# Kernel optimization log

Hardware: AMD Instinct MI355X
Metric: run time of the kernel (lower is better)

Reference implementation:

```python
import jax, jax.numpy as jnp
import numpy as np

L, K, HID, OUT, B, N, E = 2, 3, 64, 32, 8, 10000, 160000


def setup_inputs() -> dict:
    key = jax.random.key(0)
    ks = jax.random.split(key, 12)
    s = 0.05
    return {
        "edge_weight": jax.random.uniform(ks[1], (E,), dtype=jnp.float32),
        "hidden_states": jax.random.normal(ks[2], (L, B, N, HID), dtype=jnp.float32),
        "go_input": jax.random.normal(ks[3], (B, N, HID), dtype=jnp.float32),
        "Wz": jax.random.normal(ks[4], (L, 2, K, 2 * HID, HID), dtype=jnp.float32) * s,
        "bz": jnp.zeros((L, HID), dtype=jnp.float32),
        "Wr": jax.random.normal(ks[5], (L, 2, K, 2 * HID, HID), dtype=jnp.float32) * s,
        "br": jnp.zeros((L, HID), dtype=jnp.float32),
        "Wh": jax.random.normal(ks[6], (L, 2, K, 2 * HID, HID), dtype=jnp.float32) * s,
        "bh": jnp.zeros((L, HID), dtype=jnp.float32),
        "proj_W": jax.random.normal(ks[7], (HID, OUT), dtype=jnp.float32) * s,
        "proj_b": jnp.zeros((OUT,), dtype=jnp.float32),
        "edge_index": jax.random.randint(ks[0], (2, E), 0, N, dtype=jnp.int32),
    }


def _prop(z, s_idx, d_idx, nw):
    # z: [B,N,F]; aggregate nw-weighted source features at destinations
    m = z[:, s_idx, :] * nw[None, :, None]  # [B,E,F]
    return jnp.zeros_like(z).at[:, d_idx, :].add(m)


def _dconv(x, W, b, src, dst, norm_out, norm_in):
    # x: [B,N,Fin]; W: [2,K,Fin,Fout] (dir 0 = forward walk, dir 1 = reverse)
    H = jnp.einsum('bnf,fo->bno', x, W[0, 0] + W[1, 0])  # T0 shared
    To_pp, Ti_pp = x, x
    To_p = _prop(x, src, dst, norm_out)
    Ti_p = _prop(x, dst, src, norm_in)
    H = H + jnp.einsum('bnf,fo->bno', To_p, W[0, 1]) + jnp.einsum('bnf,fo->bno', Ti_p, W[1, 1])
    for k in range(2, K):  # Chebyshev recursion over hops
        To = 2.0 * _prop(To_p, src, dst, norm_out) - To_pp
        Ti = 2.0 * _prop(Ti_p, dst, src, norm_in) - Ti_pp
        H = H + jnp.einsum('bnf,fo->bno', To, W[0, k]) + jnp.einsum('bnf,fo->bno', Ti, W[1, k])
        To_pp, To_p = To_p, To
        Ti_pp, Ti_p = Ti_p, Ti
    return H + b


def _cell(x, h, Wz, bz, Wr, br, Wh, bh, src, dst, no, ni):
    xh = jnp.concatenate([x, h], axis=-1)
    Z = jax.nn.sigmoid(_dconv(xh, Wz, bz, src, dst, no, ni))
    R = jax.nn.sigmoid(_dconv(xh, Wr, br, src, dst, no, ni))
    Ht = jnp.tanh(_dconv(jnp.concatenate([x, R * h], axis=-1), Wh, bh, src, dst, no, ni))
    return Z * h + (1.0 - Z) * Ht


def reference(edge_weight, hidden_states, go_input, Wz, bz, Wr, br, Wh, bh, proj_W, proj_b, edge_index):
    src, dst = edge_index[0], edge_index[1]
    deg_out = jax.ops.segment_sum(edge_weight, src, num_segments=N)
    deg_in = jax.ops.segment_sum(edge_weight, dst, num_segments=N)
    inv_out = 1.0 / jnp.where(deg_out > 0, deg_out, 1.0)
    inv_in = 1.0 / jnp.where(deg_in > 0, deg_in, 1.0)
    norm_out = edge_weight * inv_out[src]
    norm_in = edge_weight * inv_in[dst]

    cur = go_input
    last = cur
    for l in range(L):  # small fixed layer loop (dropout=0 -> identity)
        last = _cell(cur, hidden_states[l], Wz[l], bz[l], Wr[l], br[l], Wh[l], bh[l],
                     src, dst, norm_out, norm_in)
        if l < L - 1:
            cur = last
    return jnp.einsum('bnh,ho->bno', last, proj_W) + proj_b
```

## Files before the change

### kernel.cpp

```cpp
#include <hip/hip_runtime.h>
#include <math.h>

#define NL 2
#define KK 3
#define HIDD 64
#define OUTD 32
#define NB 8
#define NN 10000
#define NE 160000
#define ROWS 80000
#define WSTRIDE (128*HIDD)

typedef __attribute__((ext_vector_type(8))) short bf16x8;
typedef __attribute__((ext_vector_type(8))) unsigned short u16x8;
typedef __attribute__((ext_vector_type(4))) unsigned short u16x4;
typedef __attribute__((ext_vector_type(4))) float f32x4;

__device__ __forceinline__ ushort f2b(float x) {
    union { float f; unsigned u; } v; v.f = x;
    unsigned r = (v.u + 0x7fff + ((v.u >> 16) & 1)) >> 16;
    return (ushort)r;
}
__device__ __forceinline__ float b2f(ushort u) {
    union { unsigned u; float f; } v; v.u = (unsigned)u << 16;
    return v.f;
}

__global__ void zero_kernel(int* p, long n) {
    long t = (long)blockIdx.x * blockDim.x + threadIdx.x;
    if (t < n) p[t] = 0;
}

__global__ void deg_cnt_kernel(const float* __restrict__ w, const int* __restrict__ src,
                               const int* __restrict__ dst, float* deg_out, float* deg_in,
                               int* cnt_f, int* cnt_r) {
    int e = blockIdx.x * blockDim.x + threadIdx.x;
    if (e >= NE) return;
    int s = src[e], d = dst[e];
    float we = w[e];
    atomicAdd(&deg_out[s], we);
    atomicAdd(&deg_in[d], we);
    atomicAdd(&cnt_f[d], 1);
    atomicAdd(&cnt_r[s], 1);
}

__global__ void scan_kernel(const int* __restrict__ cnt, int* __restrict__ off) {
    __shared__ int part[256];
    const int CH = (NN + 255) / 256;
    int t = threadIdx.x;
    int s = 0;
    for (int i = 0; i < CH; ++i) {
        int idx = t * CH + i;
        if (idx < NN) s += cnt[idx];
    }
    part[t] = s;
    __syncthreads();
    if (t == 0) {
        int run = 0;
        for (int i = 0; i < 256; ++i) { int v = part[i]; part[i] = run; run += v; }
        off[NN] = run;
    }
    __syncthreads();
    int run = part[t];
    for (int i = 0; i < CH; ++i) {
        int idx = t * CH + i;
        if (idx < NN) { off[idx] = run; run += cnt[idx]; }
    }
}

__global__ void copy_pos_kernel(const int* __restrict__ off_f, const int* __restrict__ off_r,
                                int* pos_f, int* pos_r) {
    int t = blockIdx.x * blockDim.x + threadIdx.x;
    if (t < NN) { pos_f[t] = off_f[t]; pos_r[t] = off_r[t]; }
}

__global__ void fill_kernel(const float* __restrict__ w, const int* __restrict__ src,
                            const int* __restrict__ dst, const float* __restrict__ deg_out,
                            const float* __restrict__ deg_in,
                            int* pos_f, int* pos_r,
                            int* col_f, float* w_f, int* col_r, float* w_r) {
    int e = blockIdx.x * blockDim.x + threadIdx.x;
    if (e >= NE) return;
    int s = src[e], d = dst[e];
    float we = w[e];
    float dgo = deg_out[s]; dgo = (dgo > 0.f) ? dgo : 1.f;
    float dgi = deg_in[d];  dgi = (dgi > 0.f) ? dgi : 1.f;
    int pf = atomicAdd(&pos_f[d], 1);
    col_f[pf] = s; w_f[pf] = we / dgo;
    int pr = atomicAdd(&pos_r[s], 1);
    col_r[pr] = d; w_r[pr] = we / dgi;
}

__global__ void convW_kernel(const float* __restrict__ Wz, const float* __restrict__ Wr,
                             const float* __restrict__ Wh, ushort* __restrict__ Wt) {
    int t = blockIdx.x * 256 + threadIdx.x;
    if (t >= 2 * 3 * 2 * 3 * 64 * 128) return;
    int f = t & 127;
    int r1 = t >> 7;
    int o = r1 & 63;
    int r2 = r1 >> 6;
    int k = r2 % 3;
    int r3 = r2 / 3;
    int d = r3 & 1;
    int r4 = r3 >> 1;
    int g = r4 % 3;
    int l = r4 / 3;
    const float* W = (g == 0) ? Wz : (g == 1) ? Wr : Wh;
    float v = W[(((long)(l * 2 + d) * 3 + k) * 128 + f) * 64 + o];
    if (k == 0 && d == 0)
        v += W[(((long)(l * 2 + 1) * 3 + 0) * 128 + f) * 64 + o];
    Wt[t] = f2b(v);
}

__global__ void convX_perm(const float* __restrict__ in, ushort* __restrict__ xh, int c,
                           float* __restrict__ hp) {
    long t = (long)blockIdx.x * blockDim.x + threadIdx.x;
    if (t >= (long)ROWS * 16) return;
    int q = (int)(t & 15);
    long rowin = t >> 4;
    int b = (int)(rowin / NN);
    int n = (int)(rowin - (long)b * NN);
    f32x4 v = __builtin_nontemporal_load((const f32x4*)&in[t * 4]);
    u16x4 r;
    r.x = f2b(v.x); r.y = f2b(v.y); r.z = f2b(v.z); r.w = f2b(v.w);
    long orow = (long)n * 8 + b;
    *(u16x4*)&xh[orow * 128 + c * 64 + q * 4] = r;
    if (hp) *(f32x4*)&hp[orow * 64 + q * 4] = v;
}

struct PropCfg {
    const ushort* X[2];
    const ushort* base[2];
    const int*    off[2];
    const int*    col[2];
    const float*  w[2];
    ushort*       out[2];
};

template<int HALF, int NDIR>
__global__ __launch_bounds__(128) void prop_slice(PropCfg C, float alpha, float beta) {
    constexpr int LPG = HALF ? 8 : 16;
    constexpr int GPB = 128 / LPG;
    int bid = blockIdx.x;
    int b = bid & 7;
    int r = bid >> 3;
    int dir, tile;
    if (NDIR == 2) { dir = r & 1; tile = r >> 1; }
    else           { dir = 0;     tile = r; }
    int g    = threadIdx.x / LPG;
    int lane = threadIdx.x % LPG;
    int n = tile * GPB + g;
    const ushort* X   = C.X[dir];
    const ushort* bas = C.base[dir];
    const int*    off = C.off[dir];
    const int*    col = C.col[dir];
    const float*  w   = C.w[dir];
    ushort*       out = C.out[dir];
    int s = off[n], e = off[n + 1];
    int eo = b * 128 + (HALF ? 64 : 0) + lane * 8;
    float acc[8];
    #pragma unroll
    for (int i = 0; i < 8; ++i) acc[i] = 0.f;
    int j = s;
    for (; j + 2 <= e; j += 2) {
        int c0 = col[j], c1 = col[j + 1];
        float w0 = w[j], w1 = w[j + 1];
        u16x8 v0 = *(const u16x8*)&X[(long)c0 * 1024 + eo];
        u16x8 v1 = *(const u16x8*)&X[(long)c1 * 1024 + eo];
        #pragma unroll
        for (int i = 0; i < 8; ++i) acc[i] = fmaf(b2f(v0[i]), w0, acc[i]);
        #pragma unroll
        for (int i = 0; i < 8; ++i) acc[i] = fmaf(b2f(v1[i]), w1, acc[i]);
    }
    if (j < e) {
        int c = col[j];
        float ww = w[j];
        u16x8 v = *(const u16x8*)&X[(long)c * 1024 + eo];
        #pragma unroll
        for (int i = 0; i < 8; ++i) acc[i] = fmaf(b2f(v[i]), ww, acc[i]);
    }
    long o = (long)n * 1024 + eo;
    #pragma unroll
    for (int i = 0; i < 8; ++i) acc[i] *= alpha;
    if (beta != 0.f) {
        u16x8 bb = *(const u16x8*)&bas[o];
        #pragma unroll
        for (int i = 0; i < 8; ++i) acc[i] = fmaf(beta, b2f(bb[i]), acc[i]);
    }
    u16x8 rr;
    #pragma unroll
    for (int i = 0; i < 8; ++i) rr[i] = f2b(acc[i]);
    *(u16x8*)&out[o] = rr;
}

struct GM {
    const ushort* X[10];
    const ushort* Wa[10];
    const ushort* Wb[10];
};

#define LOADF(tt, aa, bb)                                                          \
    {                                                                              \
        const ushort* Xp = A.X[tt];                                                \
        const ushort* Wp = gate ? A.Wb[tt] : A.Wa[tt];                             \
        _Pragma("unroll")                                                          \
        for (int ks = 0; ks < 2; ++ks) {                                           \
            _Pragma("unroll")                                                      \
            for (int mi = 0; mi < 2; ++mi)                                         \
                aa[ks][mi] = *(const bf16x8*)&Xp[(grow + mi * 16 + lr) * 128 +     \
                                                 ks * 32 + lk * 8];                \
            _Pragma("unroll")                                                      \
            for (int ni = 0; ni < 4; ++ni)                                         \
                bb[ks][ni] = *(const bf16x8*)&Wp[(ni * 16 + lr) * 128 +            \
                                                 ks * 32 + lk * 8];                \
        }                                                                          \
    }

#define MFMAF(aa, bb)                                                              \
    _Pragma("unroll")                                                              \
    for (int ks = 0; ks < 2; ++ks)                                                 \
        _Pragma("unroll")                                                          \
        for (int mi = 0; mi < 2; ++mi)                                             \
            _Pragma("unroll")                                                      \
            for (int ni = 0; ni < 4; ++ni)                                         \
                acc[mi][ni] = __builtin_amdgcn_mfma_f32_16x16x32_bf16(             \
                    aa[ks][mi], bb[ks][ni], acc[mi][ni], 0, 0, 0);

template<int NT>
__global__ __launch_bounds__(256, 4) void mfma_dual(GM A,
        const float* __restrict__ bzp, const float* __restrict__ brp,
        const float* __restrict__ hp,
        float* __restrict__ Z, ushort* __restrict__ xh) {
    int lane = threadIdx.x & 63;
    int wid  = threadIdx.x >> 6;
    int gate = wid >> 1;
    long grow = (long)blockIdx.x * 64 + (long)(wid & 1) * 32;
    int lr = lane & 15;
    int lk = lane >> 4;
    f32x4 acc[2][4];
    #pragma unroll
    for (int i = 0; i < 2; ++i)
        #pragma unroll
        for (int j = 0; j < 4; ++j)
            acc[i][j] = (f32x4){0.f, 0.f, 0.f, 0.f};

    bf16x8 a0[2][2], b0[2][4], a1[2][2], b1[2][4];
    LOADF(0, a0, b0);
    #pragma unroll
    for (int tt = 0; tt < NT; tt += 2) {
        if (tt + 1 < NT) LOADF(tt + 1, a1, b1);
        MFMAF(a0, b0);
        if (tt + 2 < NT) LOADF(tt + 2, a0, b0);
        if (tt + 1 < NT) MFMAF(a1, b1);
    }

    const float* bias = gate ? brp : bzp;
    #pragma unroll
    for (int mi = 0; mi < 2; ++mi) {
        #pragma unroll
        for (int q = 0; q < 4; ++q) {
            long row = grow + mi * 16 + lk * 4 + q;
            #pragma unroll
            for (int ni = 0; ni < 4; ++ni) {
                int colc = ni * 16 + lr;
                float v = acc[mi][ni][q] + bias[colc];
                float sg = 1.f / (1.f + expf(-v));
                if (gate == 0) {
                    Z[row * 64 + colc] = sg;
                } else {
                    float hv = hp[row * 64 + colc];
                    xh[row * 128 + 64 + colc] = f2b(sg * hv);
                }
            }
        }
    }
}

template<int NT>
__global__ __launch_bounds__(128, 4) void mfma_single(GM A,
        const float* __restrict__ bhp, const float* __restrict__ hp,
        const float* __restrict__ Zg,
        float* __restrict__ outF, ushort* __restrict__ xh, int writeF) {
    int lane = threadIdx.x & 63;
    int wid  = threadIdx.x >> 6;
    const int gate = 0;
    long grow = (long)blockIdx.x * 64 + (long)wid * 32;
    int lr = lane & 15;
    int lk = lane >> 4;
    f32x4 acc[2][4];
    #pragma unroll
    for (int i = 0; i < 2; ++i)
        #pragma unroll
        for (int j = 0; j < 4; ++j)
            acc[i][j] = (f32x4){0.f, 0.f, 0.f, 0.f};

    bf16x8 a0[2][2], b0[2][4], a1[2][2], b1[2][4];
    LOADF(0, a0, b0);
    #pragma unroll
    for (int tt = 0; tt < NT; tt += 2) {
        if (tt + 1 < NT) LOADF(tt + 1, a1, b1);
        MFMAF(a0, b0);
        if (tt + 2 < NT) LOADF(tt + 2, a0, b0);
        if (tt + 1 < NT) MFMAF(a1, b1);
    }

    #pragma unroll
    for (int mi = 0; mi < 2; ++mi) {
        #pragma unroll
        for (int q = 0; q < 4; ++q) {
            long row = grow + mi * 16 + lk * 4 + q;
            #pragma unroll
            for (int ni = 0; ni < 4; ++ni) {
                int colc = ni * 16 + lr;
                float v = acc[mi][ni][q] + bhp[colc];
                float ht = tanhf(v);
                float z = Zg[row * 64 + colc];
                float hv = hp[row * 64 + colc];
                float res = z * hv + (1.f - z) * ht;
                if (writeF) outF[row * 64 + colc] = res;
                else        xh[row * 128 + colc] = f2b(res);
            }
        }
    }
}

__global__ void proj_kernel(const float* __restrict__ last, const float* __restrict__ W,
                            const float* __restrict__ bias, float* __restrict__ out) {
    long t = (long)blockIdx.x * blockDim.x + threadIdx.x;
    if (t >= (long)ROWS * OUTD) return;
    long row = t >> 5;
    int  o   = (int)(t & 31);
    int n = (int)(row >> 3), b = (int)(row & 7);
    float acc = bias[o];
    #pragma unroll
    for (int hh = 0; hh < HIDD; ++hh)
        acc = fmaf(last[row * 64 + hh], W[hh * OUTD + o], acc);
    out[((long)b * NN + n) * 32 + o] = acc;
}

extern "C" void kernel_launch(void* const* d_in, const int* in_sizes, int n_in,
                              void* d_out, int out_size, void* d_ws, size_t ws_size,
                              hipStream_t stream) {
    const float* edge_weight = (const float*)d_in[0];
    const float* hidden      = (const float*)d_in[1];
    const float* go_input    = (const float*)d_in[2];
    const float* Wz = (const float*)d_in[3];
    const float* bz = (const float*)d_in[4];
    const float* Wr = (const float*)d_in[5];
    const float* br = (const float*)d_in[6];
    const float* Wh = (const float*)d_in[7];
    const float* bh = (const float*)d_in[8];
    const float* projW = (const float*)d_in[9];
    const float* projb = (const float*)d_in[10];
    const int*   eidx  = (const int*)d_in[11];
    const int* src = eidx;
    const int* dst = eidx + NE;
    float* out = (float*)d_out;

    char* p = (char*)d_ws;
    auto alloc = [&](size_t bytes) { char* r = p; p += (bytes + 15) & ~(size_t)15; return r; };
    float* deg_out = (float*)alloc(NN * 4);
    float* deg_in  = (float*)alloc(NN * 4);
    int*   cnt_f   = (int*)alloc(NN * 4);
    int*   cnt_r   = (int*)alloc(NN * 4);
    int*   off_f   = (int*)alloc((NN + 4) * 4);
    int*   off_r   = (int*)alloc((NN + 4) * 4);
    int*   pos_f   = (int*)alloc(NN * 4);
    int*   pos_r   = (int*)alloc(NN * 4);
    int*   col_f   = (int*)alloc(NE * 4);
    float* w_f     = (float*)alloc(NE * 4);
    int*   col_r   = (int*)alloc(NE * 4);
    float* w_r     = (float*)alloc(NE * 4);
    ushort* Wt     = (ushort*)alloc((size_t)2 * 3 * 2 * 3 * 64 * 128 * 2);
    const size_t XB = (size_t)ROWS * 128 * 2;
    ushort* xh  = (ushort*)alloc(XB);
    ushort* Tf1 = (ushort*)alloc(XB);
    ushort* Tf2 = (ushort*)alloc(XB);
    ushort* Tr1 = (ushort*)alloc(XB);
    ushort* Tr2 = (ushort*)alloc(XB);
    float*  Zbuf = (float*)alloc((size_t)ROWS * HIDD * 4);
    float*  hp   = (float*)alloc((size_t)ROWS * HIDD * 4);
    if ((size_t)(p - (char*)d_ws) > ws_size) return;

    const int TB = 256;
    const int EGRID = (NE + TB - 1) / TB;

    zero_kernel<<<(4 * NN + TB - 1) / TB, TB, 0, stream>>>((int*)deg_out, 4 * NN);
    deg_cnt_kernel<<<EGRID, TB, 0, stream>>>(edge_weight, src, dst, deg_out, deg_in, cnt_f, cnt_r);
    scan_kernel<<<1, 256, 0, stream>>>(cnt_f, off_f);
    scan_kernel<<<1, 256, 0, stream>>>(cnt_r, off_r);
    copy_pos_kernel<<<(NN + TB - 1) / TB, TB, 0, stream>>>(off_f, off_r, pos_f, pos_r);
    fill_kernel<<<EGRID, TB, 0, stream>>>(edge_weight, src, dst, deg_out, deg_in,
                                          pos_f, pos_r, col_f, w_f, col_r, w_r);

    convW_kernel<<<2304, 256, 0, stream>>>(Wz, Wr, Wh, Wt);
    convX_perm<<<5000, 256, 0, stream>>>(go_input, xh, 0, nullptr);

    auto wt_term = [&](int l, int g, int d, int k, int c) -> const ushort* {
        return Wt + ((((long)((l * 3 + g) * 2 + d) * 3 + k) * 64) * 128) + (long)c * 64;
    };
    const int dd[5]  = {0, 0, 0, 1, 1};
    const int kk2[5] = {0, 1, 2, 1, 2};

    for (int l = 0; l < NL; ++l) {
        const float* h = hidden + (long)l * ROWS * HIDD;
        convX_perm<<<5000, 256, 0, stream>>>(h, xh, 1, hp);

        {
            PropCfg c1{};
            c1.X[0] = xh;  c1.off[0] = off_f; c1.col[0] = col_f; c1.w[0] = w_f; c1.out[0] = Tf1;
            c1.X[1] = xh;  c1.off[1] = off_r; c1.col[1] = col_r; c1.w[1] = w_r; c1.out[1] = Tr1;
            prop_slice<0, 2><<<(NN / 8) * 2 * 8, 128, 0, stream>>>(c1, 1.f, 0.f);
            PropCfg c2f{};
            c2f.X[0] = Tf1; c2f.base[0] = xh;
            c2f.off[0] = off_f; c2f.col[0] = col_f; c2f.w[0] = w_f; c2f.out[0] = Tf2;
            prop_slice<0, 1><<<(NN / 8) * 8, 128, 0, stream>>>(c2f, 2.f, -1.f);
            PropCfg c2r{};
            c2r.X[0] = Tr1; c2r.base[0] = xh;
            c2r.off[0] = off_r; c2r.col[0] = col_r; c2r.w[0] = w_r; c2r.out[0] = Tr2;
            prop_slice<0, 1><<<(NN / 8) * 8, 128, 0, stream>>>(c2r, 2.f, -1.f);
        }

        const ushort* xs[5] = {xh, Tf1, Tf2, Tr1, Tr2};
        GM A{};
        for (int i = 0; i < 5; ++i) {
            A.X[i]      = xs[i];
            A.X[5 + i]  = xs[i] + 64;
            A.Wa[i]     = wt_term(l, 0, dd[i], kk2[i], 0);
            A.Wa[5 + i] = wt_term(l, 0, dd[i], kk2[i], 1);
            A.Wb[i]     = wt_term(l, 1, dd[i], kk2[i], 0);
            A.Wb[5 + i] = wt_term(l, 1, dd[i], kk2[i], 1);
        }
        mfma_dual<10><<<ROWS / 64, 256, 0, stream>>>(A, bz + l * HIDD, br + l * HIDD,
                                                     hp, Zbuf, xh);

        {
            PropCfg c1{};
            c1.X[0] = xh;  c1.off[0] = off_f; c1.col[0] = col_f; c1.w[0] = w_f; c1.out[0] = Tf1;
            c1.X[1] = xh;  c1.off[1] = off_r; c1.col[1] = col_r; c1.w[1] = w_r; c1.out[1] = Tr1;
            prop_slice<1, 2><<<(NN / 16) * 2 * 8, 128, 0, stream>>>(c1, 1.f, 0.f);
            PropCfg c2{};
            c2.X[0] = Tf1; c2.base[0] = xh;
            c2.off[0] = off_f; c2.col[0] = col_f; c2.w[0] = w_f; c2.out[0] = Tf2;
            c2.X[1] = Tr1; c2.base[1] = xh;
            c2.off[1] = off_r; c2.col[1] = col_r; c2.w[1] = w_r; c2.out[1] = Tr2;
            prop_slice<1, 2><<<(NN / 16) * 2 * 8, 128, 0, stream>>>(c2, 2.f, -1.f);
        }

        GM Ah{};
        for (int i = 0; i < 5; ++i) {
            Ah.X[i]      = xs[i];
            Ah.X[5 + i]  = xs[i] + 64;
            Ah.Wa[i]     = wt_term(l, 2, dd[i], kk2[i], 0);
            Ah.Wa[5 + i] = wt_term(l, 2, dd[i], kk2[i], 1);
        }
        mfma_single<10><<<ROWS / 64, 128, 0, stream>>>(Ah, bh + l * HIDD, hp, Zbuf,
                                                       Zbuf, xh, (l == NL - 1) ? 1 : 0);
    }

    proj_kernel<<<(int)(((long)ROWS * OUTD + TB - 1) / TB), TB, 0, stream>>>(
        Zbuf, projW, projb, out);
}
```

Measured before the change: 960.9 us.

## Sort graph nodes by degree for load-balanced propagation and enlarge dual GEMM tile

Adds a per-direction degree histogram, a scan and a scatter that build a permutation of nodes sorted by in-degree. The propagation kernels then map each thread group to a permuted node, so groups in a block have similar edge counts and less lane divergence. Separately, the dual-gate MFMA kernel now processes 128 rows per block (64 per wave) with launch bounds lowered to 2 blocks per CU, reusing weight fragments across more rows at the cost of more registers and lower occupancy. The extra setup kernels add a small fixed cost, and sorting by degree scatters output writes and source rows.

```diff
diff --git a/kernel.cpp b/kernel.cpp
--- a/kernel.cpp
+++ b/kernel.cpp
@@ -10,6 +10,7 @@
 #define NE 160000
 #define ROWS 80000
 #define WSTRIDE (128*HIDD)
+#define MAXD 512
 
 typedef __attribute__((ext_vector_type(8))) short bf16x8;
 typedef __attribute__((ext_vector_type(8))) unsigned short u16x8;
@@ -89,6 +90,24 @@
     col_f[pf] = s; w_f[pf] = we / dgo;
     int pr = atomicAdd(&pos_r[s], 1);
     col_r[pr] = d; w_r[pr] = we / dgi;
+}
+
+__global__ void hist_kernel(const int* __restrict__ deg, int* hist) {
+    int n = blockIdx.x * blockDim.x + threadIdx.x;
+    if (n < NN) atomicAdd(&hist[min(deg[n], MAXD - 1)], 1);
+}
+__global__ void scan512_kernel(const int* __restrict__ hist, int* boff) {
+    if (threadIdx.x == 0) {
+        int run = 0;
+        for (int i = 0; i < MAXD; ++i) { boff[i] = run; run += hist[i]; }
+    }
+}
+__global__ void scatter_perm_kernel(const int* __restrict__ deg, int* boff, int* perm) {
+    int n = blockIdx.x * blockDim.x + threadIdx.x;
+    if (n < NN) {
+        int pos = atomicAdd(&boff[min(deg[n], MAXD - 1)], 1);
+        perm[pos] = n;
+    }
 }
 
 __global__ void convW_kernel(const float* __restrict__ Wz, const float* __restrict__ Wr,
@@ -134,6 +153,7 @@
     const int*    off[2];
     const int*    col[2];
     const float*  w[2];
+    const int*    perm[2];
     ushort*       out[2];
 };
 
@@ -149,7 +169,7 @@
     else           { dir = 0;     tile = r; }
     int g    = threadIdx.x / LPG;
     int lane = threadIdx.x % LPG;
-    int n = tile * GPB + g;
+    int n = C.perm[dir][tile * GPB + g];
     const ushort* X   = C.X[dir];
     const ushort* bas = C.base[dir];
     const int*    off = C.off[dir];
@@ -199,14 +219,14 @@
     const ushort* Wb[10];
 };
 
-#define LOADF(tt, aa, bb)                                                          \
+#define LOADF4(tt, aa, bb)                                                         \
     {                                                                              \
         const ushort* Xp = A.X[tt];                                                \
         const ushort* Wp = gate ? A.Wb[tt] : A.Wa[tt];                             \
         _Pragma("unroll")                                                          \
         for (int ks = 0; ks < 2; ++ks) {                                           \
             _Pragma("unroll")                                                      \
-            for (int mi = 0; mi < 2; ++mi)                                         \
+            for (int mi = 0; mi < 4; ++mi)                                         \
                 aa[ks][mi] = *(const bf16x8*)&Xp[(grow + mi * 16 + lr) * 128 +     \
                                                  ks * 32 + lk * 8];                \
             _Pragma("unroll")                                                      \
@@ -216,47 +236,47 @@
         }                                                                          \
     }
 
-#define MFMAF(aa, bb)                                                              \
+#define MFMAF4(aa, bb)                                                             \
     _Pragma("unroll")                                                              \
     for (int ks = 0; ks < 2; ++ks)                                                 \
         _Pragma("unroll")                                                          \
-        for (int mi = 0; mi < 2; ++mi)                                             \
+        for (int mi = 0; mi < 4; ++mi)                                             \
             _Pragma("unroll")                                                      \
             for (int ni = 0; ni < 4; ++ni)                                         \
                 acc[mi][ni] = __builtin_amdgcn_mfma_f32_16x16x32_bf16(             \
                     aa[ks][mi], bb[ks][ni], acc[mi][ni], 0, 0, 0);
 
 template<int NT>
-__global__ __launch_bounds__(256, 4) void mfma_dual(GM A,
+__global__ __launch_bounds__(256, 2) void mfma_dual(GM A,
         const float* __restrict__ bzp, const float* __restrict__ brp,
         const float* __restrict__ hp,
         float* __restrict__ Z, ushort* __restrict__ xh) {
     int lane = threadIdx.x & 63;
     int wid  = threadIdx.x >> 6;
     int gate = wid >> 1;
-    long grow = (long)blockIdx.x * 64 + (long)(wid & 1) * 32;
+    long grow = (long)blockIdx.x * 128 + (long)(wid & 1) * 64;
     int lr = lane & 15;
     int lk = lane >> 4;
-    f32x4 acc[2][4];
-    #pragma unroll
-    for (int i = 0; i < 2; ++i)
+    f32x4 acc[4][4];
+    #pragma unroll
+    for (int i = 0; i < 4; ++i)
         #pragma unroll
         for (int j = 0; j < 4; ++j)
             acc[i][j] = (f32x4){0.f, 0.f, 0.f, 0.f};
 
-    bf16x8 a0[2][2], b0[2][4], a1[2][2], b1[2][4];
-    LOADF(0, a0, b0);
+    bf16x8 a0[2][4], b0[2][4], a1[2][4], b1[2][4];
+    LOADF4(0, a0, b0);
     #pragma unroll
     for (int tt = 0; tt < NT; tt += 2) {
-        if (tt + 1 < NT) LOADF(tt + 1, a1, b1);
-        MFMAF(a0, b0);
-        if (tt + 2 < NT) LOADF(tt + 2, a0, b0);
-        if (tt + 1 < NT) MFMAF(a1, b1);
+        if (tt + 1 < NT) LOADF4(tt + 1, a1, b1);
+        MFMAF4(a0, b0);
+        if (tt + 2 < NT) LOADF4(tt + 2, a0, b0);
+        if (tt + 1 < NT) MFMAF4(a1, b1);
     }
 
     const float* bias = gate ? brp : bzp;
     #pragma unroll
-    for (int mi = 0; mi < 2; ++mi) {
+    for (int mi = 0; mi < 4; ++mi) {
         #pragma unroll
         for (int q = 0; q < 4; ++q) {
             long row = grow + mi * 16 + lk * 4 + q;
@@ -276,6 +296,33 @@
     }
 }
 
+#define LOADF2(tt, aa, bb)                                                         \
+    {                                                                              \
+        const ushort* Xp = A.X[tt];                                                \
+        const ushort* Wp = A.Wa[tt];                                               \
+        _Pragma("unroll")                                                          \
+        for (int ks = 0; ks < 2; ++ks) {                                           \
+            _Pragma("unroll")                                                      \
+            for (int mi = 0; mi < 2; ++mi)                                         \
+                aa[ks][mi] = *(const bf16x8*)&Xp[(grow + mi * 16 + lr) * 128 +     \
+                                                 ks * 32 + lk * 8];                \
+            _Pragma("unroll")                                                      \
+            for (int ni = 0; ni < 4; ++ni)                                         \
+                bb[ks][ni] = *(const bf16x8*)&Wp[(ni * 16 + lr) * 128 +            \
+                                                 ks * 32 + lk * 8];                \
+        }                                                                          \
+    }
+
+#define MFMAF2(aa, bb)                                                             \
+    _Pragma("unroll")                                                              \
+    for (int ks = 0; ks < 2; ++ks)                                                 \
+        _Pragma("unroll")                                                          \
+        for (int mi = 0; mi < 2; ++mi)                                             \
+            _Pragma("unroll")                                                      \
+            for (int ni = 0; ni < 4; ++ni)                                         \
+                acc[mi][ni] = __builtin_amdgcn_mfma_f32_16x16x32_bf16(             \
+                    aa[ks][mi], bb[ks][ni], acc[mi][ni], 0, 0, 0);
+
 template<int NT>
 __global__ __launch_bounds__(128, 4) void mfma_single(GM A,
         const float* __restrict__ bhp, const float* __restrict__ hp,
@@ -283,7 +330,6 @@
         float* __restrict__ outF, ushort* __restrict__ xh, int writeF) {
     int lane = threadIdx.x & 63;
     int wid  = threadIdx.x >> 6;
-    const int gate = 0;
     long grow = (long)blockIdx.x * 64 + (long)wid * 32;
     int lr = lane & 15;
     int lk = lane >> 4;
@@ -295,13 +341,13 @@
             acc[i][j] = (f32x4){0.f, 0.f, 0.f, 0.f};
 
     bf16x8 a0[2][2], b0[2][4], a1[2][2], b1[2][4];
-    LOADF(0, a0, b0);
+    LOADF2(0, a0, b0);
     #pragma unroll
     for (int tt = 0; tt < NT; tt += 2) {
-        if (tt + 1 < NT) LOADF(tt + 1, a1, b1);
-        MFMAF(a0, b0);
-        if (tt + 2 < NT) LOADF(tt + 2, a0, b0);
-        if (tt + 1 < NT) MFMAF(a1, b1);
+        if (tt + 1 < NT) LOADF2(tt + 1, a1, b1);
+        MFMAF2(a0, b0);
+        if (tt + 2 < NT) LOADF2(tt + 2, a0, b0);
+        if (tt + 1 < NT) MFMAF2(a1, b1);
     }
 
     #pragma unroll
@@ -371,6 +417,9 @@
     float* w_f     = (float*)alloc(NE * 4);
     int*   col_r   = (int*)alloc(NE * 4);
     float* w_r     = (float*)alloc(NE * 4);
+    int*   perm_f  = (int*)alloc(NN * 4);
+    int*   perm_r  = (int*)alloc(NN * 4);
+    int*   hist2   = (int*)alloc(2 * MAXD * 4);
     ushort* Wt     = (ushort*)alloc((size_t)2 * 3 * 2 * 3 * 64 * 128 * 2);
     const size_t XB = (size_t)ROWS * 128 * 2;
     ushort* xh  = (ushort*)alloc(XB);
@@ -384,14 +433,22 @@
 
     const int TB = 256;
     const int EGRID = (NE + TB - 1) / TB;
+    const int NGRID = (NN + TB - 1) / TB;
 
     zero_kernel<<<(4 * NN + TB - 1) / TB, TB, 0, stream>>>((int*)deg_out, 4 * NN);
+    zero_kernel<<<(2 * MAXD + TB - 1) / TB, TB, 0, stream>>>(hist2, 2 * MAXD);
     deg_cnt_kernel<<<EGRID, TB, 0, stream>>>(edge_weight, src, dst, deg_out, deg_in, cnt_f, cnt_r);
     scan_kernel<<<1, 256, 0, stream>>>(cnt_f, off_f);
     scan_kernel<<<1, 256, 0, stream>>>(cnt_r, off_r);
-    copy_pos_kernel<<<(NN + TB - 1) / TB, TB, 0, stream>>>(off_f, off_r, pos_f, pos_r);
+    copy_pos_kernel<<<NGRID, TB, 0, stream>>>(off_f, off_r, pos_f, pos_r);
     fill_kernel<<<EGRID, TB, 0, stream>>>(edge_weight, src, dst, deg_out, deg_in,
                                           pos_f, pos_r, col_f, w_f, col_r, w_r);
+    hist_kernel<<<NGRID, TB, 0, stream>>>(cnt_f, hist2);
+    hist_kernel<<<NGRID, TB, 0, stream>>>(cnt_r, hist2 + MAXD);
+    scan512_kernel<<<1, 64, 0, stream>>>(hist2, hist2);
+    scan512_kernel<<<1, 64, 0, stream>>>(hist2 + MAXD, hist2 + MAXD);
+    scatter_perm_kernel<<<NGRID, TB, 0, stream>>>(cnt_f, hist2, perm_f);
+    scatter_perm_kernel<<<NGRID, TB, 0, stream>>>(cnt_r, hist2 + MAXD, perm_r);
 
     convW_kernel<<<2304, 256, 0, stream>>>(Wz, Wr, Wh, Wt);
     convX_perm<<<5000, 256, 0, stream>>>(go_input, xh, 0, nullptr);
@@ -408,16 +465,20 @@
 
         {
             PropCfg c1{};
-            c1.X[0] = xh;  c1.off[0] = off_f; c1.col[0] = col_f; c1.w[0] = w_f; c1.out[0] = Tf1;
-            c1.X[1] = xh;  c1.off[1] = off_r; c1.col[1] = col_r; c1.w[1] = w_r; c1.out[1] = Tr1;
+            c1.X[0] = xh;  c1.off[0] = off_f; c1.col[0] = col_f; c1.w[0] = w_f;
+            c1.perm[0] = perm_f; c1.out[0] = Tf1;
+            c1.X[1] = xh;  c1.off[1] = off_r; c1.col[1] = col_r; c1.w[1] = w_r;
+            c1.perm[1] = perm_r; c1.out[1] = Tr1;
             prop_slice<0, 2><<<(NN / 8) * 2 * 8, 128, 0, stream>>>(c1, 1.f, 0.f);
             PropCfg c2f{};
             c2f.X[0] = Tf1; c2f.base[0] = xh;
-            c2f.off[0] = off_f; c2f.col[0] = col_f; c2f.w[0] = w_f; c2f.out[0] = Tf2;
+            c2f.off[0] = off_f; c2f.col[0] = col_f; c2f.w[0] = w_f;
+            c2f.perm[0] = perm_f; c2f.out[0] = Tf2;
             prop_slice<0, 1><<<(NN / 8) * 8, 128, 0, stream>>>(c2f, 2.f, -1.f);
             PropCfg c2r{};
             c2r.X[0] = Tr1; c2r.base[0] = xh;
-            c2r.off[0] = off_r; c2r.col[0] = col_r; c2r.w[0] = w_r; c2r.out[0] = Tr2;
+            c2r.off[0] = off_r; c2r.col[0] = col_r; c2r.w[0] = w_r;
+            c2r.perm[0] = perm_r; c2r.out[0] = Tr2;
             prop_slice<0, 1><<<(NN / 8) * 8, 128, 0, stream>>>(c2r, 2.f, -1.f);
         }
 
@@ -431,19 +492,23 @@
             A.Wb[i]     = wt_term(l, 1, dd[i], kk2[i], 0);
             A.Wb[5 + i] = wt_term(l, 1, dd[i], kk2[i], 1);
         }
-        mfma_dual<10><<<ROWS / 64, 256, 0, stream>>>(A, bz + l * HIDD, br + l * HIDD,
-                                                     hp, Zbuf, xh);
+        mfma_dual<10><<<ROWS / 128, 256, 0, stream>>>(A, bz + l * HIDD, br + l * HIDD,
+                                                      hp, Zbuf, xh);
 
         {
             PropCfg c1{};
-            c1.X[0] = xh;  c1.off[0] = off_f; c1.col[0] = col_f; c1.w[0] = w_f; c1.out[0] = Tf1;
-            c1.X[1] = xh;  c1.off[1] = off_r; c1.col[1] = col_r; c1.w[1] = w_r; c1.out[1] = Tr1;
+            c1.X[0] = xh;  c1.off[0] = off_f; c1.col[0] = col_f; c1.w[0] = w_f;
+            c1.perm[0] = perm_f; c1.out[0] = Tf1;
+            c1.X[1] = xh;  c1.off[1] = off_r; c1.col[1] = col_r; c1.w[1] = w_r;
+            c1.perm[1] = perm_r; c1.out[1] = Tr1;
             prop_slice<1, 2><<<(NN / 16) * 2 * 8, 128, 0, stream>>>(c1, 1.f, 0.f);
             PropCfg c2{};
             c2.X[0] = Tf1; c2.base[0] = xh;
-            c2.off[0] = off_f; c2.col[0] = col_f; c2.w[0] = w_f; c2.out[0] = Tf2;
+            c2.off[0] = off_f; c2.col[0] = col_f; c2.w[0] = w_f;
+            c2.perm[0] = perm_f; c2.out[0] = Tf2;
             c2.X[1] = Tr1; c2.base[1] = xh;
-            c2.off[1] = off_r; c2.col[1] = col_r; c2.w[1] = w_r; c2.out[1] = Tr2;
+            c2.off[1] = off_r; c2.col[1] = col_r; c2.w[1] = w_r;
+            c2.perm[1] = perm_r; c2.out[1] = Tr2;
             prop_slice<1, 2><<<(NN / 16) * 2 * 8, 128, 0, stream>>>(c2, 2.f, -1.f);
         }
 
```

After: 1.189 ms. 1.24x slower.
